# Performance work log

Hardware: AMD Instinct MI355X
Metric: run time of the kernel (lower is better)

Reference implementation:

```python
import jax, jax.numpy as jnp
import numpy as np

N_NODES = 100000
N_EDGES = 1600000
HIDDEN = 128


def setup_inputs() -> dict:
    key = jax.random.key(0)
    k1, k2, k3 = jax.random.split(key, 3)
    pos = jax.random.normal(k1, (N_NODES, 3), dtype=jnp.float32)
    edge_index = jax.random.randint(k2, (2, N_EDGES), 0, N_NODES, dtype=jnp.int64)
    vector_features = jax.random.normal(k3, (N_NODES, 3, HIDDEN), dtype=jnp.float32)
    return {"pos": pos, "edge_index": edge_index, "vector_features": vector_features}


def reference(pos, edge_index, vector_features):
    # pos: (N,3); edge_index: (2,E); vector_features: (N,3,H) (unused by original math)
    H = vector_features.shape[-1]
    n_nodes = pos.shape[0]
    row, col = edge_index[0], edge_index[1]

    edge_vec = pos[col] - pos[row]                                  # (E,3)
    edge_dist = jnp.linalg.norm(edge_vec, axis=-1, keepdims=True) + 1e-8
    unit_vec = edge_vec / edge_dist                                 # (E,3)

    # scatter-add of unit vectors to both endpoints
    direction_units = (jnp.zeros((n_nodes, 3), dtype=pos.dtype)
                       .at[row].add(unit_vec)
                       .at[col].add(-unit_vec))                     # (N,3)

    # sum over spatial dim of du*du -> squared norm, broadcast to hidden
    angular_info = jnp.broadcast_to(
        jnp.sum(direction_units * direction_units, axis=1, keepdims=True),
        (n_nodes, H))                                               # (N,H)

    # vectorized per-edge dihedral: project v_i, v_j off the edge direction
    v_i = direction_units[row]                                      # (E,3)
    v_j = direction_units[col]                                      # (E,3)
    dot_vi = jnp.sum(v_i * unit_vec, axis=-1, keepdims=True)
    dot_vj = jnp.sum(v_j * (-unit_vec), axis=-1, keepdims=True)
    w_ij = v_i - dot_vi * unit_vec
    w_ji = v_j - dot_vj * (-unit_vec)
    dihedral_val = jnp.sum(w_ij * w_ji, axis=-1, keepdims=True)     # (E,1)
    dihedral_info = jnp.broadcast_to(dihedral_val, (edge_index.shape[1], H))

    return (angular_info, dihedral_info, direction_units)
```

## Files before the change

### kernel.cpp

```cpp
#include <hip/hip_runtime.h>
#include <math.h>

#define N_NODES 100000
#define N_EDGES 1600000
#define HIDDEN 128

#define NBINS      256
#define BIN_NODES  391
#define BIN_CAP    16384
#define A_THREADS  1024
#define A_EPT      2
#define A_EPB      (A_THREADS * A_EPT)
#define A_BLOCKS   ((N_EDGES + A_EPB - 1) / A_EPB)
#define B_THREADS  1024


typedef float vfloat4 __attribute__((ext_vector_type(4)));

__global__ void zero_cursors_kernel(unsigned* __restrict__ cur) {
    cur[threadIdx.x] = 0u;
}

__global__ __launch_bounds__(A_THREADS) void bin_edges_kernel(
    const int* __restrict__ eidx,
    unsigned* __restrict__ cursors,
    unsigned* __restrict__ region)
{
    __shared__ unsigned cnt[NBINS];
    __shared__ unsigned base[NBINS];
    if (threadIdx.x < NBINS) cnt[threadIdx.x] = 0u;
    __syncthreads();

    const int e0 = blockIdx.x * A_EPB + threadIdx.x * 2;
    const bool valid = (e0 < N_EDGES);

    unsigned r[A_EPT], c[A_EPT], br[A_EPT], bc[A_EPT], orow[A_EPT], ocol[A_EPT];

    if (valid) {
        int2 rr = *reinterpret_cast<const int2*>(eidx + e0);
        int2 cc = *reinterpret_cast<const int2*>(eidx + N_EDGES + e0);
        r[0] = (unsigned)rr.x; r[1] = (unsigned)rr.y;
        c[0] = (unsigned)cc.x; c[1] = (unsigned)cc.y;
        #pragma unroll
        for (int k = 0; k < A_EPT; ++k) {
            br[k] = r[k] / BIN_NODES;
            bc[k] = c[k] / BIN_NODES;
            orow[k] = atomicAdd(&cnt[br[k]], 1u);
            ocol[k] = atomicAdd(&cnt[bc[k]], 1u);
        }
    }
    __syncthreads();

    if (threadIdx.x < NBINS)
        base[threadIdx.x] = atomicAdd(&cursors[threadIdx.x], cnt[threadIdx.x]);
    __syncthreads();

    if (valid) {
        #pragma unroll
        for (int k = 0; k < A_EPT; ++k) {
            region[br[k] * BIN_CAP + base[br[k]] + orow[k]] =
                ((r[k] - br[k] * BIN_NODES) << 17) | c[k];
            region[bc[k] * BIN_CAP + base[bc[k]] + ocol[k]] =
                ((c[k] - bc[k] * BIN_NODES) << 17) | r[k];
        }
    }
}

__device__ __forceinline__ void proc_rec(unsigned rec,
                                         const float* __restrict__ posLDS,
                                         const float* __restrict__ pos,
                                         float* __restrict__ acc) {
    unsigned other = rec & 0x1FFFFu;
    unsigned local = rec >> 17;
    float sx = posLDS[local * 3 + 0];
    float sy = posLDS[local * 3 + 1];
    float sz = posLDS[local * 3 + 2];
    float dx = pos[other * 3 + 0] - sx;
    float dy = pos[other * 3 + 1] - sy;
    float dz = pos[other * 3 + 2] - sz;
    float inv = 1.0f / (sqrtf(dx * dx + dy * dy + dz * dz) + 1e-8f);
    atomicAdd(&acc[local * 3 + 0], dx * inv);
    atomicAdd(&acc[local * 3 + 1], dy * inv);
    atomicAdd(&acc[local * 3 + 2], dz * inv);
}

__global__ __launch_bounds__(B_THREADS) void accumulate_kernel(
    const float* __restrict__ pos,
    const unsigned* __restrict__ cursors,
    const unsigned* __restrict__ region,
    float* __restrict__ du,
    float* __restrict__ ang)
{
    __shared__ float acc[BIN_NODES * 3];
    __shared__ float posLDS[BIN_NODES * 3];
    const unsigned b = blockIdx.x;
    const unsigned nodebase = b * BIN_NODES;
    const unsigned nloc = min((unsigned)BIN_NODES,
                              (unsigned)(N_NODES - nodebase));

    for (int i = threadIdx.x; i < BIN_NODES * 3; i += B_THREADS) acc[i] = 0.0f;
    for (unsigned i = threadIdx.x; i < nloc * 3; i += B_THREADS)
        posLDS[i] = pos[(size_t)nodebase * 3 + i];
    __syncthreads();

    const unsigned n = cursors[b];
    const unsigned* __restrict__ reg = region + (size_t)b * BIN_CAP;
    const unsigned n4 = n & ~3u;

    for (unsigned i = threadIdx.x * 4; i < n4; i += B_THREADS * 4) {
        uint4 rc = *reinterpret_cast<const uint4*>(reg + i);
        proc_rec(rc.x, posLDS, pos, acc);
        proc_rec(rc.y, posLDS, pos, acc);
        proc_rec(rc.z, posLDS, pos, acc);
        proc_rec(rc.w, posLDS, pos, acc);
    }
    for (unsigned i = n4 + threadIdx.x; i < n; i += B_THREADS)
        proc_rec(reg[i], posLDS, pos, acc);
    __syncthreads();

    for (unsigned i = threadIdx.x; i < nloc * 3; i += B_THREADS)
        du[(size_t)nodebase * 3 + i] = acc[i];

    for (unsigned j = threadIdx.x; j < nloc * 32; j += B_THREADS) {
        unsigned node = j >> 5, c4 = j & 31;
        float x = acc[node * 3 + 0];
        float y = acc[node * 3 + 1];
        float z = acc[node * 3 + 2];
        float a = x * x + y * y + z * z;
        vfloat4 v4 = {a, a, a, a};
        __builtin_nontemporal_store(v4,
            reinterpret_cast<vfloat4*>(ang + (size_t)(nodebase + node) * HIDDEN) + c4);
    }
}

__global__ void dihedral_kernel(const float* __restrict__ pos,
                                const int* __restrict__ eidx,
                                const float* __restrict__ du,
                                float* __restrict__ dih) {
    __shared__ float vals[256];
    const int e0 = blockIdx.x * 256;
    const int e  = e0 + threadIdx.x;

    {
        int r = eidx[e];
        int c = eidx[N_EDGES + e];

        float dx = pos[c * 3 + 0] - pos[r * 3 + 0];
        float dy = pos[c * 3 + 1] - pos[r * 3 + 1];
        float dz = pos[c * 3 + 2] - pos[r * 3 + 2];
        float dist = sqrtf(dx * dx + dy * dy + dz * dz) + 1e-8f;
        float inv = 1.0f / dist;
        float ux = dx * inv, uy = dy * inv, uz = dz * inv;

        float vix = du[r * 3 + 0], viy = du[r * 3 + 1], viz = du[r * 3 + 2];
        float vjx = du[c * 3 + 0], vjy = du[c * 3 + 1], vjz = du[c * 3 + 2];

        float dvi = vix * ux + viy * uy + viz * uz;
        float dvj = -(vjx * ux + vjy * uy + vjz * uz);

        float wix = vix - dvi * ux;
        float wiy = viy - dvi * uy;
        float wiz = viz - dvi * uz;
        float wjx = vjx + dvj * ux;
        float wjy = vjy + dvj * uy;
        float wjz = vjz + dvj * uz;

        vals[threadIdx.x] = wix * wjx + wiy * wjy + wiz * wjz;
    }
    __syncthreads();

    vfloat4* out = reinterpret_cast<vfloat4*>(dih + (size_t)e0 * HIDDEN);
    #pragma unroll
    for (int it = 0; it < 32; ++it) {
        int i = it * 256 + threadIdx.x;
        float v = vals[i >> 5];
        vfloat4 v4 = {v, v, v, v};
        __builtin_nontemporal_store(v4, out + i);
    }
}

__global__ void zero_du_kernel(float* __restrict__ du, int n) {
    int i = blockIdx.x * blockDim.x + threadIdx.x;
    if (i < n) du[i] = 0.0f;
}

__global__ void edge_scatter_kernel(const float* __restrict__ pos,
                                    const int* __restrict__ eidx,
                                    float* __restrict__ du) {
    int e = blockIdx.x * blockDim.x + threadIdx.x;
    if (e >= N_EDGES) return;
    int r = eidx[e];
    int c = eidx[N_EDGES + e];
    float dx = pos[c * 3 + 0] - pos[r * 3 + 0];
    float dy = pos[c * 3 + 1] - pos[r * 3 + 1];
    float dz = pos[c * 3 + 2] - pos[r * 3 + 2];
    float inv = 1.0f / (sqrtf(dx * dx + dy * dy + dz * dz) + 1e-8f);
    float ux = dx * inv, uy = dy * inv, uz = dz * inv;
    atomicAdd(&du[r * 3 + 0],  ux);
    atomicAdd(&du[r * 3 + 1],  uy);
    atomicAdd(&du[r * 3 + 2],  uz);
    atomicAdd(&du[c * 3 + 0], -ux);
    atomicAdd(&du[c * 3 + 1], -uy);
    atomicAdd(&du[c * 3 + 2], -uz);
}

__global__ void angular_kernel(const float* __restrict__ du,
                               float* __restrict__ ang) {
    int gid = blockIdx.x * blockDim.x + threadIdx.x;
    int node = gid >> 5;
    int c4   = gid & 31;
    float x = du[node * 3 + 0];
    float y = du[node * 3 + 1];
    float z = du[node * 3 + 2];
    float a = x * x + y * y + z * z;
    vfloat4 v4 = {a, a, a, a};
    __builtin_nontemporal_store(v4,
        reinterpret_cast<vfloat4*>(ang + (size_t)node * HIDDEN) + c4);
}

extern "C" void kernel_launch(void* const* d_in, const int* in_sizes, int n_in,
                              void* d_out, int out_size, void* d_ws, size_t ws_size,
                              hipStream_t stream) {
    const float* pos  = (const float*)d_in[0];
    const int*   eidx = (const int*)d_in[1];

    float* out = (float*)d_out;
    float* ang = out;
    float* dih = out + (size_t)N_NODES * HIDDEN;
    float* du  = dih + (size_t)N_EDGES * HIDDEN;

    const size_t need = 1024 + (size_t)NBINS * BIN_CAP * sizeof(unsigned);

    if (ws_size >= need) {
        unsigned* cursors = (unsigned*)d_ws;
        unsigned* region  = (unsigned*)d_ws + 256;

        zero_cursors_kernel<<<1, NBINS, 0, stream>>>(cursors);
        bin_edges_kernel<<<A_BLOCKS, A_THREADS, 0, stream>>>(eidx, cursors, region);
        accumulate_kernel<<<NBINS, B_THREADS, 0, stream>>>(pos, cursors,
                                                           region, du, ang);
    } else {
        zero_du_kernel<<<(N_NODES * 3 + 255) / 256, 256, 0, stream>>>(du, N_NODES * 3);
        edge_scatter_kernel<<<(N_EDGES + 255) / 256, 256, 0, stream>>>(pos, eidx, du);
        angular_kernel<<<(N_NODES * 32) / 256, 256, 0, stream>>>(du, ang);
    }

    dihedral_kernel<<<N_EDGES / 256, 256, 0, stream>>>(pos, eidx, du, dih);
}
```

Measured before the change: 256.6 us.

## Use fixed-point integer LDS atomics and pad global bin cursors

The per-bin LDS accumulation switches from float atomicAdd to integer atomicAdd on values scaled by 2^22, then converts back to float when writing du and the angular output. This is meant to avoid slow float LDS atomics, possibly CAS loops. Global bin cursors are spread onto separate 128-byte lines to reduce contention on the atomic bump. BIN_CAP shrinks so the workspace fits, the fallback path uses unsafeAtomicAdd, and the dihedral kernel gets launch bounds. Fixed-point rounding adds small precision error and carries an overflow risk.

```diff
diff --git a/kernel.cpp b/kernel.cpp
--- a/kernel.cpp
+++ b/kernel.cpp
@@ -7,18 +7,22 @@
 
 #define NBINS      256
 #define BIN_NODES  391
-#define BIN_CAP    16384
+#define BIN_CAP    16256
+#define CUR_STRIDE 32
 #define A_THREADS  1024
 #define A_EPT      2
 #define A_EPB      (A_THREADS * A_EPT)
 #define A_BLOCKS   ((N_EDGES + A_EPB - 1) / A_EPB)
 #define B_THREADS  1024
 
+#define FP_SCALE   4194304.0f
+#define FP_INV     (1.0f / 4194304.0f)
+
 
 typedef float vfloat4 __attribute__((ext_vector_type(4)));
 
 __global__ void zero_cursors_kernel(unsigned* __restrict__ cur) {
-    cur[threadIdx.x] = 0u;
+    cur[threadIdx.x * CUR_STRIDE] = 0u;
 }
 
 __global__ __launch_bounds__(A_THREADS) void bin_edges_kernel(
@@ -52,7 +56,8 @@
     __syncthreads();
 
     if (threadIdx.x < NBINS)
-        base[threadIdx.x] = atomicAdd(&cursors[threadIdx.x], cnt[threadIdx.x]);
+        base[threadIdx.x] =
+            atomicAdd(&cursors[threadIdx.x * CUR_STRIDE], cnt[threadIdx.x]);
     __syncthreads();
 
     if (valid) {
@@ -69,7 +74,7 @@
 __device__ __forceinline__ void proc_rec(unsigned rec,
                                          const float* __restrict__ posLDS,
                                          const float* __restrict__ pos,
-                                         float* __restrict__ acc) {
+                                         int* __restrict__ acc) {
     unsigned other = rec & 0x1FFFFu;
     unsigned local = rec >> 17;
     float sx = posLDS[local * 3 + 0];
@@ -79,9 +84,9 @@
     float dy = pos[other * 3 + 1] - sy;
     float dz = pos[other * 3 + 2] - sz;
     float inv = 1.0f / (sqrtf(dx * dx + dy * dy + dz * dz) + 1e-8f);
-    atomicAdd(&acc[local * 3 + 0], dx * inv);
-    atomicAdd(&acc[local * 3 + 1], dy * inv);
-    atomicAdd(&acc[local * 3 + 2], dz * inv);
+    atomicAdd(&acc[local * 3 + 0], __float2int_rn(dx * inv * FP_SCALE));
+    atomicAdd(&acc[local * 3 + 1], __float2int_rn(dy * inv * FP_SCALE));
+    atomicAdd(&acc[local * 3 + 2], __float2int_rn(dz * inv * FP_SCALE));
 }
 
 __global__ __launch_bounds__(B_THREADS) void accumulate_kernel(
@@ -91,19 +96,19 @@
     float* __restrict__ du,
     float* __restrict__ ang)
 {
-    __shared__ float acc[BIN_NODES * 3];
+    __shared__ int   acc[BIN_NODES * 3];
     __shared__ float posLDS[BIN_NODES * 3];
     const unsigned b = blockIdx.x;
     const unsigned nodebase = b * BIN_NODES;
     const unsigned nloc = min((unsigned)BIN_NODES,
                               (unsigned)(N_NODES - nodebase));
 
-    for (int i = threadIdx.x; i < BIN_NODES * 3; i += B_THREADS) acc[i] = 0.0f;
+    for (int i = threadIdx.x; i < BIN_NODES * 3; i += B_THREADS) acc[i] = 0;
     for (unsigned i = threadIdx.x; i < nloc * 3; i += B_THREADS)
         posLDS[i] = pos[(size_t)nodebase * 3 + i];
     __syncthreads();
 
-    const unsigned n = cursors[b];
+    const unsigned n = cursors[b * CUR_STRIDE];
     const unsigned* __restrict__ reg = region + (size_t)b * BIN_CAP;
     const unsigned n4 = n & ~3u;
 
@@ -119,13 +124,13 @@
     __syncthreads();
 
     for (unsigned i = threadIdx.x; i < nloc * 3; i += B_THREADS)
-        du[(size_t)nodebase * 3 + i] = acc[i];
+        du[(size_t)nodebase * 3 + i] = (float)acc[i] * FP_INV;
 
     for (unsigned j = threadIdx.x; j < nloc * 32; j += B_THREADS) {
         unsigned node = j >> 5, c4 = j & 31;
-        float x = acc[node * 3 + 0];
-        float y = acc[node * 3 + 1];
-        float z = acc[node * 3 + 2];
+        float x = (float)acc[node * 3 + 0] * FP_INV;
+        float y = (float)acc[node * 3 + 1] * FP_INV;
+        float z = (float)acc[node * 3 + 2] * FP_INV;
         float a = x * x + y * y + z * z;
         vfloat4 v4 = {a, a, a, a};
         __builtin_nontemporal_store(v4,
@@ -133,10 +138,12 @@
     }
 }
 
-__global__ void dihedral_kernel(const float* __restrict__ pos,
-                                const int* __restrict__ eidx,
-                                const float* __restrict__ du,
-                                float* __restrict__ dih) {
+__global__ __launch_bounds__(256) void dihedral_kernel(
+    const float* __restrict__ pos,
+    const int* __restrict__ eidx,
+    const float* __restrict__ du,
+    float* __restrict__ dih)
+{
     __shared__ float vals[256];
     const int e0 = blockIdx.x * 256;
     const int e  = e0 + threadIdx.x;
@@ -196,12 +203,12 @@
     float dz = pos[c * 3 + 2] - pos[r * 3 + 2];
     float inv = 1.0f / (sqrtf(dx * dx + dy * dy + dz * dz) + 1e-8f);
     float ux = dx * inv, uy = dy * inv, uz = dz * inv;
-    atomicAdd(&du[r * 3 + 0],  ux);
-    atomicAdd(&du[r * 3 + 1],  uy);
-    atomicAdd(&du[r * 3 + 2],  uz);
-    atomicAdd(&du[c * 3 + 0], -ux);
-    atomicAdd(&du[c * 3 + 1], -uy);
-    atomicAdd(&du[c * 3 + 2], -uz);
+    unsafeAtomicAdd(&du[r * 3 + 0],  ux);
+    unsafeAtomicAdd(&du[r * 3 + 1],  uy);
+    unsafeAtomicAdd(&du[r * 3 + 2],  uz);
+    unsafeAtomicAdd(&du[c * 3 + 0], -ux);
+    unsafeAtomicAdd(&du[c * 3 + 1], -uy);
+    unsafeAtomicAdd(&du[c * 3 + 2], -uz);
 }
 
 __global__ void angular_kernel(const float* __restrict__ du,
@@ -229,11 +236,12 @@
     float* dih = out + (size_t)N_NODES * HIDDEN;
     float* du  = dih + (size_t)N_EDGES * HIDDEN;
 
-    const size_t need = 1024 + (size_t)NBINS * BIN_CAP * sizeof(unsigned);
+    const size_t curBytes = (size_t)NBINS * CUR_STRIDE * sizeof(unsigned);
+    const size_t need = curBytes + (size_t)NBINS * BIN_CAP * sizeof(unsigned);
 
     if (ws_size >= need) {
         unsigned* cursors = (unsigned*)d_ws;
-        unsigned* region  = (unsigned*)d_ws + 256;
+        unsigned* region  = (unsigned*)d_ws + NBINS * CUR_STRIDE;
 
         zero_cursors_kernel<<<1, NBINS, 0, stream>>>(cursors);
         bin_edges_kernel<<<A_BLOCKS, A_THREADS, 0, stream>>>(eidx, cursors, region);
```

After: 217.8 us. 1.18x faster.
